# Performance work log

Measured on AMD Instinct MI355X. Metric: run time of the kernel, lower is better.

## Reference

```python
import jax, jax.numpy as jnp
import numpy as np

N_AGENTS = 32
STATE_DIM = 6 * N_AGENTS      # 192
CONTROL_DIM = 3 * N_AGENTS    # 96
HIDDEN = 100
NEWTON_ITERS = 40

# Index maps from the cvxpy objective:
#   p[u_x_r]^T u[u_idx] + p[u_y_r]^T u[2*u_idx] + p[u_z_r]^T u[3*u_idx]
_u_idx = np.arange(N_AGENTS)
P_IDX = np.concatenate([3 * np.arange(1, N_AGENTS + 1),
                        4 * np.arange(1, N_AGENTS + 1),
                        5 * np.arange(1, N_AGENTS + 1)])
U_IDX = np.concatenate([_u_idx, 2 * _u_idx, 3 * _u_idx])


def _p_net(t, z, W1, b1, W2, b2, W3, b3):
    # DefaultPNet: MLP on concat([t, z]) with tanh hiddens (hidden_dim=100)
    x = jnp.concatenate([t, z], axis=-1)          # [B, 1+STATE_DIM]
    h = jnp.tanh(x @ W1 + b1)
    h = jnp.tanh(h @ W2 + b2)
    return h @ W3 + b3                            # [B, STATE_DIM]


def _solve_qp(q):
    # min_u q^T u + 0.5||u||^2 + 0.25||u||^4  (unconstrained, strictly convex)
    # Stationarity: q + (1+||u||^2) u = 0 => u = -q/(1+s), s = ||u||^2
    # => s (1+s)^2 = ||q||^2 ; solve scalar cubic per row via Newton.
    r = jnp.sum(q * q, axis=-1)                   # [B]
    s0 = jnp.cbrt(r)                              # good init: s ~ r^(1/3) for large r

    def step(s, _):
        one = 1.0 + s
        f = s * one * one - r
        fp = one * one + 2.0 * s * one
        return jnp.maximum(s - f / fp, 0.0), None

    s, _ = jax.lax.scan(step, s0, None, length=NEWTON_ITERS)
    return -q / (1.0 + s)[:, None]                # [B, CONTROL_DIM]


def setup_inputs() -> dict:
    key = jax.random.key(0)
    ks = jax.random.split(key, 8)
    B = 131072
    in_dim = 1 + STATE_DIM
    sc1 = 1.0 / np.sqrt(in_dim)
    sc2 = 1.0 / np.sqrt(HIDDEN)
    return {
        "z": jax.random.normal(ks[0], (B, STATE_DIM), jnp.float32),
        "t": jax.random.uniform(ks[1], (B, 1), jnp.float32),
        "W1": jax.random.normal(ks[2], (in_dim, HIDDEN), jnp.float32) * sc1,
        "b1": jnp.zeros((HIDDEN,), jnp.float32),
        "W2": jax.random.normal(ks[3], (HIDDEN, HIDDEN), jnp.float32) * sc2,
        "b2": jnp.zeros((HIDDEN,), jnp.float32),
        "W3": jax.random.normal(ks[4], (HIDDEN, STATE_DIM), jnp.float32) * sc2,
        "b3": jnp.zeros((STATE_DIM,), jnp.float32),
    }


def reference(z, t, W1, b1, W2, b2, W3, b3):
    p = _p_net(t, z, W1, b1, W2, b2, W3, b3)      # [B, STATE_DIM]
    # Accumulate linear coefficients onto u (indices overlap, so scatter-add)
    q = jnp.zeros((p.shape[0], CONTROL_DIM), p.dtype).at[:, U_IDX].add(p[:, P_IDX])
    return _solve_qp(q)                            # ustar [B, CONTROL_DIM]
```

## Files before the change

kernel.cpp:

```cpp
#include <hip/hip_runtime.h>
#include <hip/hip_bf16.h>


typedef __attribute__((ext_vector_type(8))) short short8;
typedef __attribute__((ext_vector_type(4))) short short4v;
typedef __attribute__((ext_vector_type(4))) float f32x4;

#define HST 116

__device__ __forceinline__ unsigned short f2bf(float f) {
  unsigned u = __float_as_uint(f);
  u += 0x7fffu + ((u >> 16) & 1u);
  return (unsigned short)(u >> 16);
}
__device__ __forceinline__ float tanh_fast(float x) {
  float ax = fabsf(x);
  float e = __builtin_amdgcn_exp2f(ax * -2.88539008177792681f);
  float r = (1.f - e) * __builtin_amdgcn_rcpf(1.f + e);
  return copysignf(r, x);
}

__global__ void cvx_prep(const float* __restrict__ W1, const float* __restrict__ b1,
                         const float* __restrict__ W2, const float* __restrict__ b2,
                         const float* __restrict__ W3, const float* __restrict__ b3,
                         short* __restrict__ pw) {
  int idx = blockIdx.x * 256 + threadIdx.x;

  if (idx < 21504) {
    int kt = idx / 3584, rem = idx % 3584;
    int nt = rem / 512, e = rem % 512;
    int lane = e >> 3, j = e & 7;
    int k = kt * 32 + (lane >> 4) * 8 + j;
    int n = nt * 16 + (lane & 15);
    float wv = (n < 100) ? W1[(k + 1) * 100 + n] : 0.f;
    pw[(kt * 7 + nt) * 512 + e] = (short)f2bf(wv);
    return;
  }
  idx -= 21504;
  if (idx < 14336) {
    int kt = idx / 3584, rem = idx % 3584;
    int nt = rem / 512, e = rem % 512;
    int lane = e >> 3, j = e & 7;
    int k = kt * 32 + (lane >> 4) * 8 + j;
    int n = nt * 16 + (lane & 15);
    float wv = (k < 100 && n < 100) ? W2[k * 100 + n] : 0.f;
    pw[21504 + (kt * 7 + nt) * 512 + e] = (short)f2bf(wv);
    return;
  }
  idx -= 14336;
  if (idx < 12288) {
    int kt = idx / 3072, rem = idx % 3072;
    int nt = rem / 512, e = rem % 512;
    int lane = e >> 3, j = e & 7;
    int k = kt * 32 + (lane >> 4) * 8 + j;
    int u = nt * 16 + (lane & 15);
    float wv = 0.f;
    if (k < 100) {
      const float* wr = W3 + k * 192;
      if (u <= 31) wv += wr[3 * u + 3];
      if ((u & 1) == 0 && u <= 62) wv += wr[2 * u + 4];
      if (u % 3 == 0 && u <= 93) wv += wr[(5 * u) / 3 + 5];
    }
    pw[35840 + (kt * 6 + nt) * 512 + e] = (short)f2bf(wv);
    return;
  }
  idx -= 12288;
  float* cb = (float*)(pw + 48128);
  if (idx < 112) { cb[idx] = (idx < 100) ? W1[idx] : 0.f; return; }
  idx -= 112;
  if (idx < 112) { cb[112 + idx] = (idx < 100) ? b1[idx] : 0.f; return; }
  idx -= 112;
  if (idx < 112) { cb[224 + idx] = (idx < 100) ? b2[idx] : 0.f; return; }
  idx -= 112;
  if (idx < 96) {
    int u = idx;
    float v = 0.f;
    if (u <= 31) v += b3[3 * u + 3];
    if ((u & 1) == 0 && u <= 62) v += b3[2 * u + 4];
    if (u % 3 == 0 && u <= 93) v += b3[(5 * u) / 3 + 5];
    cb[336 + u] = v;
  }
}

__global__ __launch_bounds__(1024) void cvx_main(
    const float* __restrict__ zin, const float* __restrict__ tin,
    const short* __restrict__ pw, float* __restrict__ out) {
  __shared__ __align__(16) short wbuf[48128];
  __shared__ __align__(16) short hbuf[16 * 16 * HST];

  const int tid = threadIdx.x;
  const int wid = tid >> 6;
  const int lane = tid & 63;
  const int l15 = lane & 15;
  const int qd = lane >> 4;

  for (int f = wid; f < 94; f += 16) {
    const short* g = pw + f * 512 + lane * 8;
    __builtin_amdgcn_global_load_lds(
        (const __attribute__((address_space(1))) void*)g,
        (__attribute__((address_space(3))) void*)&wbuf[f * 512], 16, 0, 0);
  }

  const int rb = blockIdx.x * 256 + wid * 16;
  const int hb = wid * 16 * HST;
  const float* cb = (const float*)(pw + 48128);

  short8 XA[6];
  float tcur;
  {
    const float* zr = zin + (size_t)(rb + l15) * 192 + qd * 8;
    f32x4 za[6], zb[6];
#pragma unroll
    for (int kt = 0; kt < 6; kt++) {
      za[kt] = *(const f32x4*)(zr + kt * 32);
      zb[kt] = *(const f32x4*)(zr + kt * 32 + 4);
    }
    tcur = tin[rb + l15];
#pragma unroll
    for (int kt = 0; kt < 6; kt++) {
      union { short8 s; __hip_bfloat162 h[4]; } u;
      u.h[0] = __float22bfloat162_rn(make_float2(za[kt][0], za[kt][1]));
      u.h[1] = __float22bfloat162_rn(make_float2(za[kt][2], za[kt][3]));
      u.h[2] = __float22bfloat162_rn(make_float2(zb[kt][0], zb[kt][1]));
      u.h[3] = __float22bfloat162_rn(make_float2(zb[kt][2], zb[kt][3]));
      XA[kt] = u.s;
    }
  }

  __syncthreads();

  auto ldh = [&](int off) -> short8 {
    short4v a = *(const short4v*)&hbuf[off];
    short4v b = *(const short4v*)&hbuf[off + 4];
    return __builtin_shufflevector(a, b, 0, 1, 2, 3, 4, 5, 6, 7);
  };

  f32x4 acc[7];
#pragma unroll
  for (int nt = 0; nt < 7; nt++) { f32x4 z4 = {0.f, 0.f, 0.f, 0.f}; acc[nt] = z4; }
#pragma unroll
  for (int kt = 0; kt < 6; kt++)
#pragma unroll
    for (int nt = 0; nt < 7; nt++) {
      short8 bf = *(const short8*)&wbuf[(kt * 7 + nt) * 512 + lane * 8];
      acc[nt] = __builtin_amdgcn_mfma_f32_16x16x32_bf16(XA[kt], bf, acc[nt], 0, 0, 0);
    }
  float tr[4];
#pragma unroll
  for (int r = 0; r < 4; r++) tr[r] = __shfl(tcur, qd * 4 + r);
#pragma unroll
  for (int nt = 0; nt < 7; nt++) {
    float w0n = cb[nt * 16 + l15];
    float b1n = cb[112 + nt * 16 + l15];
#pragma unroll
    for (int r = 0; r < 4; r++) {
      float v = fmaf(tr[r], w0n, acc[nt][r] + b1n);
      hbuf[hb + (qd * 4 + r) * HST + nt * 16 + l15] = (short)f2bf(tanh_fast(v));
    }
  }

  short8 HA[4];
  {
    int ro = hb + l15 * HST;
#pragma unroll
    for (int kt = 0; kt < 3; kt++) HA[kt] = ldh(ro + kt * 32 + qd * 8);
    HA[3] = ldh(ro + 96 + (qd & 1) * 8);
  }
#pragma unroll
  for (int nt = 0; nt < 7; nt++) { f32x4 z4 = {0.f, 0.f, 0.f, 0.f}; acc[nt] = z4; }
#pragma unroll
  for (int kt = 0; kt < 4; kt++)
#pragma unroll
    for (int nt = 0; nt < 7; nt++) {
      short8 bf = *(const short8*)&wbuf[(42 + kt * 7 + nt) * 512 + lane * 8];
      acc[nt] = __builtin_amdgcn_mfma_f32_16x16x32_bf16(HA[kt], bf, acc[nt], 0, 0, 0);
    }
#pragma unroll
  for (int nt = 0; nt < 7; nt++) {
    float b2n = cb[224 + nt * 16 + l15];
#pragma unroll
    for (int r = 0; r < 4; r++)
      hbuf[hb + (qd * 4 + r) * HST + nt * 16 + l15] = (short)f2bf(tanh_fast(acc[nt][r] + b2n));
  }

  {
    int ro = hb + l15 * HST;
#pragma unroll
    for (int kt = 0; kt < 3; kt++) HA[kt] = ldh(ro + kt * 32 + qd * 8);
    HA[3] = ldh(ro + 96 + (qd & 1) * 8);
  }
  f32x4 qa[6];
#pragma unroll
  for (int nt = 0; nt < 6; nt++) { f32x4 z4 = {0.f, 0.f, 0.f, 0.f}; qa[nt] = z4; }
#pragma unroll
  for (int kt = 0; kt < 4; kt++)
#pragma unroll
    for (int nt = 0; nt < 6; nt++) {
      short8 bf = *(const short8*)&wbuf[(70 + kt * 6 + nt) * 512 + lane * 8];
      qa[nt] = __builtin_amdgcn_mfma_f32_16x16x32_bf16(HA[kt], bf, qa[nt], 0, 0, 0);
    }

#pragma unroll
  for (int nt = 0; nt < 6; nt++) {
    float bq = cb[336 + nt * 16 + l15];
    qa[nt][0] += bq; qa[nt][1] += bq; qa[nt][2] += bq; qa[nt][3] += bq;
  }
  f32x4 rs = {0.f, 0.f, 0.f, 0.f};
#pragma unroll
  for (int nt = 0; nt < 6; nt++) rs += qa[nt] * qa[nt];
  float rv[4];
#pragma unroll
  for (int r = 0; r < 4; r++) {
    float v = rs[r];
    v += __shfl_xor(v, 1);
    v += __shfl_xor(v, 2);
    v += __shfl_xor(v, 4);
    v += __shfl_xor(v, 8);
    rv[r] = v;
  }
  float r2 = rv[l15 & 3];
  float s = __builtin_amdgcn_exp2f(__builtin_amdgcn_logf(r2) * 0.333333333333f);
#pragma unroll
  for (int itn = 0; itn < 8; itn++) {
    float one = 1.f + s;
    float fv = fmaf(s * one, one, -r2);
    float fp = one * fmaf(2.f, s, one);
    s = fmaxf(s - fv * __builtin_amdgcn_rcpf(fp), 0.f);
  }
  float myinv = -__builtin_amdgcn_rcpf(1.f + s);
#pragma unroll
  for (int r = 0; r < 4; r++) {
    float inv = __shfl(myinv, (lane & 48) | r);
    float* orow = out + (size_t)(rb + qd * 4 + r) * 96;
#pragma unroll
    for (int nt = 0; nt < 6; nt++)
      orow[nt * 16 + l15] = qa[nt][r] * inv;
  }
}

extern "C" void kernel_launch(void* const* d_in, const int* in_sizes, int n_in,
                              void* d_out, int out_size, void* d_ws, size_t ws_size,
                              hipStream_t stream) {
  const float* z  = (const float*)d_in[0];
  const float* t  = (const float*)d_in[1];
  const float* W1 = (const float*)d_in[2];
  const float* b1 = (const float*)d_in[3];
  const float* W2 = (const float*)d_in[4];
  const float* b2 = (const float*)d_in[5];
  const float* W3 = (const float*)d_in[6];
  const float* b3 = (const float*)d_in[7];
  float* out = (float*)d_out;
  int B = in_sizes[0] / 192;

  short* pw = (short*)d_ws;
  cvx_prep<<<190, 256, 0, stream>>>(W1, b1, W2, b2, W3, b3, pw);
  cvx_main<<<B / 256, 1024, 0, stream>>>(z, t, pw, out);
}
```

Measured before the change: 193.4 us.

## Read MLP weights straight from global memory instead of staging in LDS

Drops the per-block copy of the ~94KB packed bf16 weights into shared memory and the block-wide barrier. Each MFMA now reads its B-fragment directly from global memory, relying on L1/L2 caching. Blocks shrink from 1024 to 256 threads, so more blocks fit per CU with less LDS. The z loads and output stores also become nontemporal. The cost is that every weight access is now a global load with higher latency instead of an LDS read.

```diff
diff --git a/kernel.cpp b/kernel.cpp
--- a/kernel.cpp
+++ b/kernel.cpp
@@ -82,11 +82,10 @@
   }
 }
 
-__global__ __launch_bounds__(1024) void cvx_main(
+__global__ __launch_bounds__(256) void cvx_main(
     const float* __restrict__ zin, const float* __restrict__ tin,
     const short* __restrict__ pw, float* __restrict__ out) {
-  __shared__ __align__(16) short wbuf[48128];
-  __shared__ __align__(16) short hbuf[16 * 16 * HST];
+  __shared__ __align__(16) short hbuf[4 * 16 * HST];
 
   const int tid = threadIdx.x;
   const int wid = tid >> 6;
@@ -94,14 +93,7 @@
   const int l15 = lane & 15;
   const int qd = lane >> 4;
 
-  for (int f = wid; f < 94; f += 16) {
-    const short* g = pw + f * 512 + lane * 8;
-    __builtin_amdgcn_global_load_lds(
-        (const __attribute__((address_space(1))) void*)g,
-        (__attribute__((address_space(3))) void*)&wbuf[f * 512], 16, 0, 0);
-  }
-
-  const int rb = blockIdx.x * 256 + wid * 16;
+  const int rb = blockIdx.x * 64 + wid * 16;
   const int hb = wid * 16 * HST;
   const float* cb = (const float*)(pw + 48128);
 
@@ -112,8 +104,8 @@
     f32x4 za[6], zb[6];
 #pragma unroll
     for (int kt = 0; kt < 6; kt++) {
-      za[kt] = *(const f32x4*)(zr + kt * 32);
-      zb[kt] = *(const f32x4*)(zr + kt * 32 + 4);
+      za[kt] = __builtin_nontemporal_load((const f32x4*)(zr + kt * 32));
+      zb[kt] = __builtin_nontemporal_load((const f32x4*)(zr + kt * 32 + 4));
     }
     tcur = tin[rb + l15];
 #pragma unroll
@@ -127,8 +119,9 @@
     }
   }
 
-  __syncthreads();
-
+  auto ldw = [&](int f) -> short8 {
+    return *(const short8*)(pw + f * 512 + lane * 8);
+  };
   auto ldh = [&](int off) -> short8 {
     short4v a = *(const short4v*)&hbuf[off];
     short4v b = *(const short4v*)&hbuf[off + 4];
@@ -141,10 +134,8 @@
 #pragma unroll
   for (int kt = 0; kt < 6; kt++)
 #pragma unroll
-    for (int nt = 0; nt < 7; nt++) {
-      short8 bf = *(const short8*)&wbuf[(kt * 7 + nt) * 512 + lane * 8];
-      acc[nt] = __builtin_amdgcn_mfma_f32_16x16x32_bf16(XA[kt], bf, acc[nt], 0, 0, 0);
-    }
+    for (int nt = 0; nt < 7; nt++)
+      acc[nt] = __builtin_amdgcn_mfma_f32_16x16x32_bf16(XA[kt], ldw(kt * 7 + nt), acc[nt], 0, 0, 0);
   float tr[4];
 #pragma unroll
   for (int r = 0; r < 4; r++) tr[r] = __shfl(tcur, qd * 4 + r);
@@ -171,10 +162,8 @@
 #pragma unroll
   for (int kt = 0; kt < 4; kt++)
 #pragma unroll
-    for (int nt = 0; nt < 7; nt++) {
-      short8 bf = *(const short8*)&wbuf[(42 + kt * 7 + nt) * 512 + lane * 8];
-      acc[nt] = __builtin_amdgcn_mfma_f32_16x16x32_bf16(HA[kt], bf, acc[nt], 0, 0, 0);
-    }
+    for (int nt = 0; nt < 7; nt++)
+      acc[nt] = __builtin_amdgcn_mfma_f32_16x16x32_bf16(HA[kt], ldw(42 + kt * 7 + nt), acc[nt], 0, 0, 0);
 #pragma unroll
   for (int nt = 0; nt < 7; nt++) {
     float b2n = cb[224 + nt * 16 + l15];
@@ -195,10 +184,8 @@
 #pragma unroll
   for (int kt = 0; kt < 4; kt++)
 #pragma unroll
-    for (int nt = 0; nt < 6; nt++) {
-      short8 bf = *(const short8*)&wbuf[(70 + kt * 6 + nt) * 512 + lane * 8];
-      qa[nt] = __builtin_amdgcn_mfma_f32_16x16x32_bf16(HA[kt], bf, qa[nt], 0, 0, 0);
-    }
+    for (int nt = 0; nt < 6; nt++)
+      qa[nt] = __builtin_amdgcn_mfma_f32_16x16x32_bf16(HA[kt], ldw(70 + kt * 6 + nt), qa[nt], 0, 0, 0);
 
 #pragma unroll
   for (int nt = 0; nt < 6; nt++) {
@@ -234,7 +221,7 @@
     float* orow = out + (size_t)(rb + qd * 4 + r) * 96;
 #pragma unroll
     for (int nt = 0; nt < 6; nt++)
-      orow[nt * 16 + l15] = qa[nt][r] * inv;
+      __builtin_nontemporal_store(qa[nt][r] * inv, &orow[nt * 16 + l15]);
   }
 }
 
@@ -254,5 +241,5 @@
 
   short* pw = (short*)d_ws;
   cvx_prep<<<190, 256, 0, stream>>>(W1, b1, W2, b2, W3, b3, pw);
-  cvx_main<<<B / 256, 1024, 0, stream>>>(z, t, pw, out);
-}
+  cvx_main<<<B / 64, 256, 0, stream>>>(z, t, pw, out);
+}
```

Result: slower. 203.2 us (+5.1%).

## Process two row tiles per block with prefetch of next tile's inputs

Applied to the files above, without the earlier changes.

Each block now handles 512 rows in two sequential passes, and the launch uses half as many blocks. The roughly 96KB weight load into LDS is amortized over twice the rows. While the first tile's layer-1 MFMAs run, the next tile's z and t values are loaded from global memory into registers. Hidden-state stores are also rewritten to use packed bf16 conversion. The cost is more live registers and fewer blocks, which may reduce occupancy or leave tail imbalance across CUs.

```diff
diff --git a/kernel.cpp b/kernel.cpp
--- a/kernel.cpp
+++ b/kernel.cpp
@@ -101,21 +101,44 @@
         (__attribute__((address_space(3))) void*)&wbuf[f * 512], 16, 0, 0);
   }
 
-  const int rb = blockIdx.x * 256 + wid * 16;
+  const int r0 = blockIdx.x * 512 + wid * 16;
   const int hb = wid * 16 * HST;
   const float* cb = (const float*)(pw + 48128);
 
-  short8 XA[6];
+  f32x4 za[6], zb[6];
   float tcur;
   {
-    const float* zr = zin + (size_t)(rb + l15) * 192 + qd * 8;
-    f32x4 za[6], zb[6];
+    const float* zr = zin + (size_t)(r0 + l15) * 192 + qd * 8;
 #pragma unroll
     for (int kt = 0; kt < 6; kt++) {
       za[kt] = *(const f32x4*)(zr + kt * 32);
       zb[kt] = *(const f32x4*)(zr + kt * 32 + 4);
     }
-    tcur = tin[rb + l15];
+    tcur = tin[r0 + l15];
+  }
+
+  __syncthreads();
+
+  auto ldh = [&](int off) -> short8 {
+    short4v a = *(const short4v*)&hbuf[off];
+    short4v b = *(const short4v*)&hbuf[off + 4];
+    return __builtin_shufflevector(a, b, 0, 1, 2, 3, 4, 5, 6, 7);
+  };
+  auto sth = [&](int col, float v0, float v1, float v2, float v3) {
+    union { __hip_bfloat162 h; unsigned u; } p0, p1;
+    p0.h = __float22bfloat162_rn(make_float2(v0, v1));
+    p1.h = __float22bfloat162_rn(make_float2(v2, v3));
+    hbuf[hb + (qd * 4 + 0) * HST + col] = (short)(p0.u & 0xffff);
+    hbuf[hb + (qd * 4 + 1) * HST + col] = (short)(p0.u >> 16);
+    hbuf[hb + (qd * 4 + 2) * HST + col] = (short)(p1.u & 0xffff);
+    hbuf[hb + (qd * 4 + 3) * HST + col] = (short)(p1.u >> 16);
+  };
+
+#pragma unroll 1
+  for (int g = 0; g < 2; ++g) {
+    const int rb = r0 + g * 256;
+
+    short8 XA[6];
 #pragma unroll
     for (int kt = 0; kt < 6; kt++) {
       union { short8 s; __hip_bfloat162 h[4]; } u;
@@ -125,116 +148,122 @@
       u.h[3] = __float22bfloat162_rn(make_float2(zb[kt][2], zb[kt][3]));
       XA[kt] = u.s;
     }
-  }
-
-  __syncthreads();
-
-  auto ldh = [&](int off) -> short8 {
-    short4v a = *(const short4v*)&hbuf[off];
-    short4v b = *(const short4v*)&hbuf[off + 4];
-    return __builtin_shufflevector(a, b, 0, 1, 2, 3, 4, 5, 6, 7);
-  };
-
-  f32x4 acc[7];
-#pragma unroll
-  for (int nt = 0; nt < 7; nt++) { f32x4 z4 = {0.f, 0.f, 0.f, 0.f}; acc[nt] = z4; }
-#pragma unroll
-  for (int kt = 0; kt < 6; kt++)
+    const float tnow = tcur;
+
+    f32x4 acc[7];
+#pragma unroll
+    for (int nt = 0; nt < 7; nt++) { f32x4 z4 = {0.f, 0.f, 0.f, 0.f}; acc[nt] = z4; }
+#pragma unroll
+    for (int kt = 0; kt < 6; kt++)
+#pragma unroll
+      for (int nt = 0; nt < 7; nt++) {
+        short8 bf = *(const short8*)&wbuf[(kt * 7 + nt) * 512 + lane * 8];
+        acc[nt] = __builtin_amdgcn_mfma_f32_16x16x32_bf16(XA[kt], bf, acc[nt], 0, 0, 0);
+      }
+
+    if (g == 0) {
+      const float* zr = zin + (size_t)(r0 + 256 + l15) * 192 + qd * 8;
+#pragma unroll
+      for (int kt = 0; kt < 6; kt++) {
+        za[kt] = *(const f32x4*)(zr + kt * 32);
+        zb[kt] = *(const f32x4*)(zr + kt * 32 + 4);
+      }
+      tcur = tin[r0 + 256 + l15];
+    }
+
+    float tr[4];
+#pragma unroll
+    for (int r = 0; r < 4; r++) tr[r] = __shfl(tnow, qd * 4 + r);
 #pragma unroll
     for (int nt = 0; nt < 7; nt++) {
-      short8 bf = *(const short8*)&wbuf[(kt * 7 + nt) * 512 + lane * 8];
-      acc[nt] = __builtin_amdgcn_mfma_f32_16x16x32_bf16(XA[kt], bf, acc[nt], 0, 0, 0);
-    }
-  float tr[4];
-#pragma unroll
-  for (int r = 0; r < 4; r++) tr[r] = __shfl(tcur, qd * 4 + r);
-#pragma unroll
-  for (int nt = 0; nt < 7; nt++) {
-    float w0n = cb[nt * 16 + l15];
-    float b1n = cb[112 + nt * 16 + l15];
+      float w0n = cb[nt * 16 + l15];
+      float b1n = cb[112 + nt * 16 + l15];
+      float h[4];
+#pragma unroll
+      for (int r = 0; r < 4; r++)
+        h[r] = tanh_fast(fmaf(tr[r], w0n, acc[nt][r] + b1n));
+      sth(nt * 16 + l15, h[0], h[1], h[2], h[3]);
+    }
+
+    short8 HA[4];
+    {
+      int ro = hb + l15 * HST;
+#pragma unroll
+      for (int kt = 0; kt < 3; kt++) HA[kt] = ldh(ro + kt * 32 + qd * 8);
+      HA[3] = ldh(ro + 96 + (qd & 1) * 8);
+    }
+#pragma unroll
+    for (int nt = 0; nt < 7; nt++) { f32x4 z4 = {0.f, 0.f, 0.f, 0.f}; acc[nt] = z4; }
+#pragma unroll
+    for (int kt = 0; kt < 4; kt++)
+#pragma unroll
+      for (int nt = 0; nt < 7; nt++) {
+        short8 bf = *(const short8*)&wbuf[(42 + kt * 7 + nt) * 512 + lane * 8];
+        acc[nt] = __builtin_amdgcn_mfma_f32_16x16x32_bf16(HA[kt], bf, acc[nt], 0, 0, 0);
+      }
+#pragma unroll
+    for (int nt = 0; nt < 7; nt++) {
+      float b2n = cb[224 + nt * 16 + l15];
+      float h[4];
+#pragma unroll
+      for (int r = 0; r < 4; r++)
+        h[r] = tanh_fast(acc[nt][r] + b2n);
+      sth(nt * 16 + l15, h[0], h[1], h[2], h[3]);
+    }
+
+    {
+      int ro = hb + l15 * HST;
+#pragma unroll
+      for (int kt = 0; kt < 3; kt++) HA[kt] = ldh(ro + kt * 32 + qd * 8);
+      HA[3] = ldh(ro + 96 + (qd & 1) * 8);
+    }
+    f32x4 qa[6];
+#pragma unroll
+    for (int nt = 0; nt < 6; nt++) { f32x4 z4 = {0.f, 0.f, 0.f, 0.f}; qa[nt] = z4; }
+#pragma unroll
+    for (int kt = 0; kt < 4; kt++)
+#pragma unroll
+      for (int nt = 0; nt < 6; nt++) {
+        short8 bf = *(const short8*)&wbuf[(70 + kt * 6 + nt) * 512 + lane * 8];
+        qa[nt] = __builtin_amdgcn_mfma_f32_16x16x32_bf16(HA[kt], bf, qa[nt], 0, 0, 0);
+      }
+
+#pragma unroll
+    for (int nt = 0; nt < 6; nt++) {
+      float bq = cb[336 + nt * 16 + l15];
+      qa[nt][0] += bq; qa[nt][1] += bq; qa[nt][2] += bq; qa[nt][3] += bq;
+    }
+    f32x4 rs = {0.f, 0.f, 0.f, 0.f};
+#pragma unroll
+    for (int nt = 0; nt < 6; nt++) rs += qa[nt] * qa[nt];
+    float rv[4];
 #pragma unroll
     for (int r = 0; r < 4; r++) {
-      float v = fmaf(tr[r], w0n, acc[nt][r] + b1n);
-      hbuf[hb + (qd * 4 + r) * HST + nt * 16 + l15] = (short)f2bf(tanh_fast(v));
-    }
-  }
-
-  short8 HA[4];
-  {
-    int ro = hb + l15 * HST;
-#pragma unroll
-    for (int kt = 0; kt < 3; kt++) HA[kt] = ldh(ro + kt * 32 + qd * 8);
-    HA[3] = ldh(ro + 96 + (qd & 1) * 8);
-  }
-#pragma unroll
-  for (int nt = 0; nt < 7; nt++) { f32x4 z4 = {0.f, 0.f, 0.f, 0.f}; acc[nt] = z4; }
-#pragma unroll
-  for (int kt = 0; kt < 4; kt++)
-#pragma unroll
-    for (int nt = 0; nt < 7; nt++) {
-      short8 bf = *(const short8*)&wbuf[(42 + kt * 7 + nt) * 512 + lane * 8];
-      acc[nt] = __builtin_amdgcn_mfma_f32_16x16x32_bf16(HA[kt], bf, acc[nt], 0, 0, 0);
-    }
-#pragma unroll
-  for (int nt = 0; nt < 7; nt++) {
-    float b2n = cb[224 + nt * 16 + l15];
-#pragma unroll
-    for (int r = 0; r < 4; r++)
-      hbuf[hb + (qd * 4 + r) * HST + nt * 16 + l15] = (short)f2bf(tanh_fast(acc[nt][r] + b2n));
-  }
-
-  {
-    int ro = hb + l15 * HST;
-#pragma unroll
-    for (int kt = 0; kt < 3; kt++) HA[kt] = ldh(ro + kt * 32 + qd * 8);
-    HA[3] = ldh(ro + 96 + (qd & 1) * 8);
-  }
-  f32x4 qa[6];
-#pragma unroll
-  for (int nt = 0; nt < 6; nt++) { f32x4 z4 = {0.f, 0.f, 0.f, 0.f}; qa[nt] = z4; }
-#pragma unroll
-  for (int kt = 0; kt < 4; kt++)
-#pragma unroll
-    for (int nt = 0; nt < 6; nt++) {
-      short8 bf = *(const short8*)&wbuf[(70 + kt * 6 + nt) * 512 + lane * 8];
-      qa[nt] = __builtin_amdgcn_mfma_f32_16x16x32_bf16(HA[kt], bf, qa[nt], 0, 0, 0);
-    }
-
-#pragma unroll
-  for (int nt = 0; nt < 6; nt++) {
-    float bq = cb[336 + nt * 16 + l15];
-    qa[nt][0] += bq; qa[nt][1] += bq; qa[nt][2] += bq; qa[nt][3] += bq;
-  }
-  f32x4 rs = {0.f, 0.f, 0.f, 0.f};
-#pragma unroll
-  for (int nt = 0; nt < 6; nt++) rs += qa[nt] * qa[nt];
-  float rv[4];
-#pragma unroll
-  for (int r = 0; r < 4; r++) {
-    float v = rs[r];
-    v += __shfl_xor(v, 1);
-    v += __shfl_xor(v, 2);
-    v += __shfl_xor(v, 4);
-    v += __shfl_xor(v, 8);
-    rv[r] = v;
-  }
-  float r2 = rv[l15 & 3];
-  float s = __builtin_amdgcn_exp2f(__builtin_amdgcn_logf(r2) * 0.333333333333f);
-#pragma unroll
-  for (int itn = 0; itn < 8; itn++) {
-    float one = 1.f + s;
-    float fv = fmaf(s * one, one, -r2);
-    float fp = one * fmaf(2.f, s, one);
-    s = fmaxf(s - fv * __builtin_amdgcn_rcpf(fp), 0.f);
-  }
-  float myinv = -__builtin_amdgcn_rcpf(1.f + s);
-#pragma unroll
-  for (int r = 0; r < 4; r++) {
-    float inv = __shfl(myinv, (lane & 48) | r);
-    float* orow = out + (size_t)(rb + qd * 4 + r) * 96;
-#pragma unroll
-    for (int nt = 0; nt < 6; nt++)
-      orow[nt * 16 + l15] = qa[nt][r] * inv;
+      float v = rs[r];
+      v += __shfl_xor(v, 1);
+      v += __shfl_xor(v, 2);
+      v += __shfl_xor(v, 4);
+      v += __shfl_xor(v, 8);
+      rv[r] = v;
+    }
+    float r2 = rv[l15 & 3];
+    float s = __builtin_amdgcn_exp2f(__builtin_amdgcn_logf(r2) * 0.333333333333f);
+#pragma unroll
+    for (int itn = 0; itn < 8; itn++) {
+      float one = 1.f + s;
+      float fv = fmaf(s * one, one, -r2);
+      float fp = one * fmaf(2.f, s, one);
+      s = fmaxf(s - fv * __builtin_amdgcn_rcpf(fp), 0.f);
+    }
+    float myinv = -__builtin_amdgcn_rcpf(1.f + s);
+#pragma unroll
+    for (int r = 0; r < 4; r++) {
+      float inv = __shfl(myinv, (lane & 48) | r);
+      float* orow = out + (size_t)(rb + qd * 4 + r) * 96;
+#pragma unroll
+      for (int nt = 0; nt < 6; nt++)
+        orow[nt * 16 + l15] = qa[nt][r] * inv;
+    }
   }
 }
 
@@ -254,5 +283,5 @@
 
   short* pw = (short*)d_ws;
   cvx_prep<<<190, 256, 0, stream>>>(W1, b1, W2, b2, W3, b3, pw);
-  cvx_main<<<B / 256, 1024, 0, stream>>>(z, t, pw, out);
-}
+  cvx_main<<<B / 512, 1024, 0, stream>>>(z, t, pw, out);
+}
```

Measured after the change: 276.8 us. 1.43x slower.
